# Optimization experiments

Hardware: AMD Instinct MI355X
Metric: run time of the kernel (lower is better)

## Reference

```python
import jax, jax.numpy as jnp
import numpy as np

B, S, H, N = 2, 2048, 1024, 16
D = H // N


def setup_inputs() -> dict:
    key = jax.random.key(0)
    k1, k2, k3 = jax.random.split(key, 3)
    # Xavier-uniform-ish init for projection weights
    lim_in = (6.0 / (H + 3 * H)) ** 0.5
    lim_out = (6.0 / (H + H)) ** 0.5
    return {
        "hidden_states": jax.random.normal(k1, (B, S, H), dtype=jnp.float32),
        "w_in": jax.random.uniform(k2, (3 * H, H), minval=-lim_in, maxval=lim_in, dtype=jnp.float32),
        "b_in": jnp.zeros((3 * H,), dtype=jnp.float32),
        "w_out": jax.random.uniform(k3, (H, H), minval=-lim_out, maxval=lim_out, dtype=jnp.float32),
        "b_out": jnp.zeros((H,), dtype=jnp.float32),
    }


def reference(hidden_states, w_in, b_in, w_out, b_out):
    b, s, h = hidden_states.shape
    qkv = hidden_states @ w_in.T + b_in  # [B,S,3H]
    q, k, v = jnp.split(qkv, 3, axis=-1)
    # [B,S,H] -> [B,N,S,D]
    def to_heads(x):
        return x.reshape(b, s, N, D).transpose(0, 2, 1, 3)
    q, k, v = to_heads(q), to_heads(k), to_heads(v)
    scale = D ** -0.5
    scores = jnp.einsum("bnqd,bnkd->bnqk", q, k) * scale  # [B,N,S,S]
    causal = jnp.triu(jnp.ones((s, s), dtype=bool), k=1)
    scores = jnp.where(causal, -jnp.inf, scores)
    attn = jax.nn.softmax(scores, axis=-1)
    out = jnp.einsum("bnqk,bnkd->bnqd", attn, v)  # [B,N,S,D]
    out = out.transpose(0, 2, 1, 3).reshape(b, s, h)
    return out @ w_out.T + b_out
```

## Files before the change

kernel.cpp:

```cpp
#include <hip/hip_runtime.h>
#include <hip/hip_bf16.h>

#define BB 2
#define SS 2048
#define HH 1024
#define NH 16
#define DD 64
#define H3 3072
#define MM (BB*SS)

typedef unsigned short u16;
typedef unsigned int u32;
typedef __attribute__((ext_vector_type(8))) short bf16x8;
typedef __attribute__((ext_vector_type(4))) float f32x4;

__device__ __forceinline__ u16 f2bf(float f) {
    union { float f; u32 u; } v; v.f = f;
    u32 u = v.u;
    u += 0x7fffu + ((u >> 16) & 1u);
    return (u16)(u >> 16);
}
__device__ __forceinline__ float bf2f(u16 h) {
    union { u32 u; float f; } v; v.u = ((u32)h) << 16;
    return v.f;
}
__device__ __forceinline__ u32 pack2bf(float a, float b) {
    __hip_bfloat162 h = __float22bfloat162_rn(float2{a, b});
    u32 u; __builtin_memcpy(&u, &h, 4);
    return u;
}
__device__ __forceinline__ void gl_lds16(const void* g, void* l) {
    __builtin_amdgcn_global_load_lds(
        (const __attribute__((address_space(1))) u32*)g,
        (__attribute__((address_space(3))) u32*)l, 16, 0, 0);
}

__global__ void cvt2bf(const float4* __restrict__ s0, uint2* __restrict__ d0, int n0,
                       const float4* __restrict__ s1, uint2* __restrict__ d1, int n1) {
    int i = blockIdx.x * blockDim.x + threadIdx.x;
    const int tot = n0 + n1;
    for (; i < tot; i += gridDim.x * blockDim.x) {
        const float4* s = (i < n0) ? s0 : s1;
        uint2* d       = (i < n0) ? d0 : d1;
        int j          = (i < n0) ? i : i - n0;
        float4 v = s[j];
        uint2 o; o.x = pack2bf(v.x, v.y); o.y = pack2bf(v.z, v.w);
        d[j] = o;
    }
}

template<bool ACVT, int BN, int MODE>
__global__ __launch_bounds__(256, 2)
void gemm_k(const void* __restrict__ Aptr, const u16* __restrict__ Bbf,
            const u16* __restrict__ biasbf, void* __restrict__ Cptr,
            u16* __restrict__ qk, u16* __restrict__ vt, int M, int Nn, int K)
{
    constexpr int ASTR = ACVT ? 40 : 32;
    constexpr int NFR  = BN / 32;
    __shared__ __align__(16) u16 Alds[128 * ASTR];
    __shared__ __align__(16) u16 Blds[BN * 32];
    const int tid = threadIdx.x;
    const int w = tid >> 6, lane = tid & 63, quad = lane >> 4, l16 = lane & 15;
    const int m0 = blockIdx.x * 128, n0 = blockIdx.y * BN;
    const int wm = w >> 1, wn = w & 1;
    const int rA = lane >> 3, c4 = (lane & 7) * 4;
    const int rA4 = lane >> 2, c8b = (lane & 3) * 8;

    f32x4 acc[4][NFR] = {};

    for (int k0 = 0; k0 < K; k0 += 32) {
        __syncthreads();
        if constexpr (ACVT) {
            const float* A = (const float*)Aptr;
#pragma unroll
            for (int q = 0; q < 4; ++q) {
                int row = w * 32 + q * 8 + rA;
                float4 v = *(const float4*)&A[(size_t)(m0 + row) * K + k0 + c4];
                u32* dst = (u32*)&Alds[row * ASTR + c4];
                dst[0] = pack2bf(v.x, v.y);
                dst[1] = pack2bf(v.z, v.w);
            }
        } else {
            const u16* A = (const u16*)Aptr;
#pragma unroll
            for (int q = 0; q < 2; ++q) {
                int row0 = w * 32 + q * 16;
                gl_lds16(&A[(size_t)(m0 + row0 + rA4) * K + k0 + c8b],
                         &Alds[row0 * 32]);
            }
        }
#pragma unroll
        for (int q = 0; q < BN / 64; ++q) {
            int row0 = w * (BN / 4) + q * 16;
            gl_lds16(&Bbf[(size_t)(n0 + row0 + rA4) * K + k0 + c8b],
                     &Blds[row0 * 32]);
        }
        __syncthreads();

        bf16x8 af[4], bfr[NFR];
#pragma unroll
        for (int mi = 0; mi < 4; ++mi)
            af[mi] = *(const bf16x8*)&Alds[(wm * 64 + mi * 16 + l16) * ASTR + quad * 8];
#pragma unroll
        for (int ni = 0; ni < NFR; ++ni)
            bfr[ni] = *(const bf16x8*)&Blds[(wn * (BN / 2) + ni * 16 + l16) * 32 + quad * 8];
#pragma unroll
        for (int mi = 0; mi < 4; ++mi)
#pragma unroll
            for (int ni = 0; ni < NFR; ++ni)
                acc[mi][ni] = __builtin_amdgcn_mfma_f32_16x16x32_bf16(
                    af[mi], bfr[ni], acc[mi][ni], 0, 0, 0);
    }

#pragma unroll
    for (int mi = 0; mi < 4; ++mi) {
        int row_b = m0 + wm * 64 + mi * 16 + quad * 4;
#pragma unroll
        for (int ni = 0; ni < NFR; ++ni) {
            int col = n0 + wn * (BN / 2) + ni * 16 + l16;
            float bv = bf2f(biasbf[col]);
            if constexpr (MODE == 1) {
#pragma unroll
                for (int i = 0; i < 4; ++i)
                    ((float*)Cptr)[(size_t)(row_b + i) * Nn + col] = acc[mi][ni][i] + bv;
            } else {
                if (col < 2048) {
                    float sc = (col < 1024) ? 0.125f : 1.0f;
#pragma unroll
                    for (int i = 0; i < 4; ++i)
                        qk[(size_t)(row_b + i) * 2048 + col] = f2bf((acc[mi][ni][i] + bv) * sc);
                } else {
                    int d = col - 2048, hh = d >> 6, dd = d & 63;
                    int b = row_b >> 11, s = row_b & 2047;
                    u16 t0 = f2bf(acc[mi][ni][0] + bv), t1 = f2bf(acc[mi][ni][1] + bv);
                    u16 t2 = f2bf(acc[mi][ni][2] + bv), t3 = f2bf(acc[mi][ni][3] + bv);
                    uint2 pk; pk.x = (u32)t0 | ((u32)t1 << 16);
                    pk.y = (u32)t2 | ((u32)t3 << 16);
                    *(uint2*)&vt[((size_t)((b * 16 + hh) * 64 + dd)) * 2048 + s] = pk;
                }
            }
        }
    }
}

__global__ __launch_bounds__(256, 2)
void attn_v2(const u16* __restrict__ qk, const u16* __restrict__ vt,
             u16* __restrict__ attn_out) {
    const int pr = blockIdx.x, h = blockIdx.y, b = blockIdx.z;
    const int tid = threadIdx.x;
    const int w = tid >> 6, lane = tid & 63, quad = lane >> 4, l16 = lane & 15;
    __shared__ __align__(16) u16 Klds[64 * 72];
    __shared__ __align__(16) u16 Vlds[64 * 72];
    __shared__ __align__(16) u16 Pbuf[64 * 72];
    __shared__ float Lred[4][64];
    __shared__ float Linv[64];

    const int r0 = tid >> 3, cc8 = (tid & 7) * 8;

    for (int half = 0; half < 2; ++half) {
        const int qt = (half == 0) ? (31 - pr) : pr;
        const int q0 = qt * 64;
        const int T = qt + 1;

        bf16x8 qf[4][2];
        {
            const u16* qb = qk + (size_t)(b * SS + q0) * 2048 + h * 64;
#pragma unroll
            for (int mi = 0; mi < 4; ++mi)
#pragma unroll
                for (int kc = 0; kc < 2; ++kc)
                    qf[mi][kc] = *(const bf16x8*)
                        &qb[(size_t)(mi * 16 + l16) * 2048 + kc * 32 + quad * 8];
        }

        const u16* Kg = qk + (size_t)(b * SS) * 2048 + 1024 + h * 64;
        const u16* Vg = vt + (size_t)((b * 16 + h) * 64) * 2048;

        f32x4 oacc[4] = {};
        float l_lane[16];
#pragma unroll
        for (int j = 0; j < 16; ++j) l_lane[j] = 0.f;

        uint4 kr0, kr1, vr0, vr1;
        kr0 = *(const uint4*)&Kg[(size_t)(r0) * 2048 + cc8];
        kr1 = *(const uint4*)&Kg[(size_t)(r0 + 32) * 2048 + cc8];
        vr0 = *(const uint4*)&Vg[(size_t)(r0) * 2048 + cc8];
        vr1 = *(const uint4*)&Vg[(size_t)(r0 + 32) * 2048 + cc8];

        for (int t = 0; t < T; ++t) {
            const int kv0 = t * 64;
            __syncthreads();
            *(uint4*)&Klds[r0 * 72 + cc8]        = kr0;
            *(uint4*)&Klds[(r0 + 32) * 72 + cc8] = kr1;
            *(uint4*)&Vlds[r0 * 72 + cc8]        = vr0;
            *(uint4*)&Vlds[(r0 + 32) * 72 + cc8] = vr1;
            __syncthreads();
            if (t + 1 < T) {
                const int nv = kv0 + 64;
                kr0 = *(const uint4*)&Kg[(size_t)(nv + r0) * 2048 + cc8];
                kr1 = *(const uint4*)&Kg[(size_t)(nv + r0 + 32) * 2048 + cc8];
                vr0 = *(const uint4*)&Vg[(size_t)(r0) * 2048 + nv + cc8];
                vr1 = *(const uint4*)&Vg[(size_t)(r0 + 32) * 2048 + nv + cc8];
            }
            bf16x8 kf0 = *(const bf16x8*)&Klds[(w * 16 + l16) * 72 + quad * 8];
            bf16x8 kf1 = *(const bf16x8*)&Klds[(w * 16 + l16) * 72 + 32 + quad * 8];
            f32x4 sacc[4] = {};
#pragma unroll
            for (int mi = 0; mi < 4; ++mi) {
                sacc[mi] = __builtin_amdgcn_mfma_f32_16x16x32_bf16(qf[mi][0], kf0, sacc[mi], 0, 0, 0);
                sacc[mi] = __builtin_amdgcn_mfma_f32_16x16x32_bf16(qf[mi][1], kf1, sacc[mi], 0, 0, 0);
            }
            const int colg = kv0 + w * 16 + l16;
#pragma unroll
            for (int mi = 0; mi < 4; ++mi) {
#pragma unroll
                for (int i = 0; i < 4; ++i) {
                    int rowg = q0 + mi * 16 + quad * 4 + i;
                    float p = (colg <= rowg) ? __expf(sacc[mi][i]) : 0.f;
                    l_lane[mi * 4 + i] += p;
                    Pbuf[(mi * 16 + quad * 4 + i) * 72 + w * 16 + l16] = f2bf(p);
                }
            }
            __syncthreads();
            bf16x8 vf0 = *(const bf16x8*)&Vlds[(w * 16 + l16) * 72 + quad * 8];
            bf16x8 vf1 = *(const bf16x8*)&Vlds[(w * 16 + l16) * 72 + 32 + quad * 8];
#pragma unroll
            for (int mi = 0; mi < 4; ++mi) {
                bf16x8 pf0 = *(const bf16x8*)&Pbuf[(mi * 16 + l16) * 72 + quad * 8];
                bf16x8 pf1 = *(const bf16x8*)&Pbuf[(mi * 16 + l16) * 72 + 32 + quad * 8];
                oacc[mi] = __builtin_amdgcn_mfma_f32_16x16x32_bf16(pf0, vf0, oacc[mi], 0, 0, 0);
                oacc[mi] = __builtin_amdgcn_mfma_f32_16x16x32_bf16(pf1, vf1, oacc[mi], 0, 0, 0);
            }
        }

#pragma unroll
        for (int j = 0; j < 16; ++j) {
#pragma unroll
            for (int s = 1; s < 16; s <<= 1)
                l_lane[j] += __shfl_xor(l_lane[j], s, 64);
        }
#pragma unroll
        for (int j = 0; j < 16; ++j)
            if (l16 == j) Lred[w][(j >> 2) * 16 + quad * 4 + (j & 3)] = l_lane[j];
        __syncthreads();
        if (w == 0)
            Linv[lane] = 1.0f / (Lred[0][lane] + Lred[1][lane] + Lred[2][lane] + Lred[3][lane]);
        __syncthreads();
        {
            u16* ob = attn_out + (size_t)(b * SS + q0) * 1024 + h * 64 + w * 16 + l16;
#pragma unroll
            for (int mi = 0; mi < 4; ++mi)
#pragma unroll
                for (int i = 0; i < 4; ++i) {
                    int rl = mi * 16 + quad * 4 + i;
                    ob[(size_t)rl * 1024] = f2bf(oacc[mi][i] * Linv[rl]);
                }
        }
        __syncthreads();
    }
}

extern "C" void kernel_launch(void* const* d_in, const int* in_sizes, int n_in,
                              void* d_out, int out_size, void* d_ws, size_t ws_size,
                              hipStream_t stream) {
    const float* hidden = (const float*)d_in[0];
    const float* w_in   = (const float*)d_in[1];
    const float* b_in   = (const float*)d_in[2];
    const float* w_out  = (const float*)d_in[3];
    const float* b_out  = (const float*)d_in[4];
    float* out = (float*)d_out;

    char* ws = (char*)d_ws;
    u16* wi_bf   = (u16*)ws;
    u16* bi_bf   = (u16*)(ws + 6291456);
    u16* attn_ws = (u16*)ws;
    u16* qk      = (u16*)(ws + 8388608);
    u16* wo_bf   = (u16*)(ws + 8388608);
    u16* bo_bf   = (u16*)(ws + 8388608 + 2097152);
    u16* vt      = (u16*)(ws + 25165824);

    cvt2bf<<<dim3(1024), dim3(256), 0, stream>>>(
        (const float4*)w_in, (uint2*)wi_bf, 786432,
        (const float4*)b_in, (uint2*)bi_bf, 768);
    gemm_k<true, 128, 2><<<dim3(32, 24), dim3(256), 0, stream>>>(
        hidden, wi_bf, bi_bf, nullptr, qk, vt, MM, H3, HH);
    attn_v2<<<dim3(16, NH, BB), dim3(256), 0, stream>>>(qk, vt, attn_ws);
    cvt2bf<<<dim3(1024), dim3(256), 0, stream>>>(
        (const float4*)w_out, (uint2*)wo_bf, 262144,
        (const float4*)b_out, (uint2*)bo_bf, 256);
    gemm_k<false, 64, 1><<<dim3(32, 16), dim3(256), 0, stream>>>(
        attn_ws, wo_bf, bo_bf, out, nullptr, nullptr, MM, HH, HH);
}
```

Before: 189.4 us.

## Restructure attention per-wave rows with double-buffered K/V and pre-converted bf16 input

The attention kernel now gives each wave its own 16 query rows across all 64 keys. This makes the row-sum reduction wave-local, removes the cross-wave LDS reduction, and gives each wave a private P buffer, which cuts barriers per tile from two to one. K and V tiles are double-buffered in LDS so the next tile's global loads overlap compute. The hidden states are converted to bf16 up front into the output buffer, so the QKV GEMM can use the async global-to-LDS path, and Q and K are split into separate contiguous buffers. This adds an extra conversion pass and doubles K/V LDS usage.

```diff
diff --git a/kernel.cpp b/kernel.cpp
--- a/kernel.cpp
+++ b/kernel.cpp
@@ -35,72 +35,58 @@
         (__attribute__((address_space(3))) u32*)l, 16, 0, 0);
 }
 
-__global__ void cvt2bf(const float4* __restrict__ s0, uint2* __restrict__ d0, int n0,
-                       const float4* __restrict__ s1, uint2* __restrict__ d1, int n1) {
+__global__ void cvt3bf(const float4* __restrict__ s0, uint2* __restrict__ d0, int n0,
+                       const float4* __restrict__ s1, uint2* __restrict__ d1, int n1,
+                       const float4* __restrict__ s2, uint2* __restrict__ d2, int n2) {
     int i = blockIdx.x * blockDim.x + threadIdx.x;
-    const int tot = n0 + n1;
+    const int tot = n0 + n1 + n2;
     for (; i < tot; i += gridDim.x * blockDim.x) {
-        const float4* s = (i < n0) ? s0 : s1;
-        uint2* d       = (i < n0) ? d0 : d1;
-        int j          = (i < n0) ? i : i - n0;
+        const float4* s; uint2* d; int j;
+        if (i < n0)            { s = s0; d = d0; j = i; }
+        else if (i < n0 + n1)  { s = s1; d = d1; j = i - n0; }
+        else                   { s = s2; d = d2; j = i - n0 - n1; }
         float4 v = s[j];
         uint2 o; o.x = pack2bf(v.x, v.y); o.y = pack2bf(v.z, v.w);
         d[j] = o;
     }
 }
 
-template<bool ACVT, int BN, int MODE>
+template<int BN, int MODE>
 __global__ __launch_bounds__(256, 2)
-void gemm_k(const void* __restrict__ Aptr, const u16* __restrict__ Bbf,
-            const u16* __restrict__ biasbf, void* __restrict__ Cptr,
-            u16* __restrict__ qk, u16* __restrict__ vt, int M, int Nn, int K)
+void gemm_k2(const u16* __restrict__ A, const u16* __restrict__ Bbf,
+             const u16* __restrict__ biasbf, void* __restrict__ Cptr,
+             u16* __restrict__ Qo, u16* __restrict__ Ko, u16* __restrict__ Vto,
+             int M, int Nn, int K)
 {
-    constexpr int ASTR = ACVT ? 40 : 32;
-    constexpr int NFR  = BN / 32;
-    __shared__ __align__(16) u16 Alds[128 * ASTR];
+    constexpr int NFR = BN / 32;
+    __shared__ __align__(16) u16 Alds[128 * 32];
     __shared__ __align__(16) u16 Blds[BN * 32];
     const int tid = threadIdx.x;
     const int w = tid >> 6, lane = tid & 63, quad = lane >> 4, l16 = lane & 15;
     const int m0 = blockIdx.x * 128, n0 = blockIdx.y * BN;
     const int wm = w >> 1, wn = w & 1;
-    const int rA = lane >> 3, c4 = (lane & 7) * 4;
     const int rA4 = lane >> 2, c8b = (lane & 3) * 8;
 
     f32x4 acc[4][NFR] = {};
 
     for (int k0 = 0; k0 < K; k0 += 32) {
         __syncthreads();
-        if constexpr (ACVT) {
-            const float* A = (const float*)Aptr;
-#pragma unroll
-            for (int q = 0; q < 4; ++q) {
-                int row = w * 32 + q * 8 + rA;
-                float4 v = *(const float4*)&A[(size_t)(m0 + row) * K + k0 + c4];
-                u32* dst = (u32*)&Alds[row * ASTR + c4];
-                dst[0] = pack2bf(v.x, v.y);
-                dst[1] = pack2bf(v.z, v.w);
-            }
-        } else {
-            const u16* A = (const u16*)Aptr;
-#pragma unroll
-            for (int q = 0; q < 2; ++q) {
-                int row0 = w * 32 + q * 16;
-                gl_lds16(&A[(size_t)(m0 + row0 + rA4) * K + k0 + c8b],
-                         &Alds[row0 * 32]);
-            }
+#pragma unroll
+        for (int q = 0; q < 2; ++q) {
+            int row0 = w * 32 + q * 16;
+            gl_lds16(&A[(size_t)(m0 + row0 + rA4) * K + k0 + c8b], &Alds[row0 * 32]);
         }
 #pragma unroll
         for (int q = 0; q < BN / 64; ++q) {
             int row0 = w * (BN / 4) + q * 16;
-            gl_lds16(&Bbf[(size_t)(n0 + row0 + rA4) * K + k0 + c8b],
-                     &Blds[row0 * 32]);
+            gl_lds16(&Bbf[(size_t)(n0 + row0 + rA4) * K + k0 + c8b], &Blds[row0 * 32]);
         }
         __syncthreads();
 
         bf16x8 af[4], bfr[NFR];
 #pragma unroll
         for (int mi = 0; mi < 4; ++mi)
-            af[mi] = *(const bf16x8*)&Alds[(wm * 64 + mi * 16 + l16) * ASTR + quad * 8];
+            af[mi] = *(const bf16x8*)&Alds[(wm * 64 + mi * 16 + l16) * 32 + quad * 8];
 #pragma unroll
         for (int ni = 0; ni < NFR; ++ni)
             bfr[ni] = *(const bf16x8*)&Blds[(wn * (BN / 2) + ni * 16 + l16) * 32 + quad * 8];
@@ -124,11 +110,16 @@
                 for (int i = 0; i < 4; ++i)
                     ((float*)Cptr)[(size_t)(row_b + i) * Nn + col] = acc[mi][ni][i] + bv;
             } else {
-                if (col < 2048) {
-                    float sc = (col < 1024) ? 0.125f : 1.0f;
+                if (col < 1024) {
 #pragma unroll
                     for (int i = 0; i < 4; ++i)
-                        qk[(size_t)(row_b + i) * 2048 + col] = f2bf((acc[mi][ni][i] + bv) * sc);
+                        Qo[(size_t)(row_b + i) * 1024 + col] =
+                            f2bf((acc[mi][ni][i] + bv) * 0.125f);
+                } else if (col < 2048) {
+#pragma unroll
+                    for (int i = 0; i < 4; ++i)
+                        Ko[(size_t)(row_b + i) * 1024 + (col - 1024)] =
+                            f2bf(acc[mi][ni][i] + bv);
                 } else {
                     int d = col - 2048, hh = d >> 6, dd = d & 63;
                     int b = row_b >> 11, s = row_b & 2047;
@@ -136,7 +127,7 @@
                     u16 t2 = f2bf(acc[mi][ni][2] + bv), t3 = f2bf(acc[mi][ni][3] + bv);
                     uint2 pk; pk.x = (u32)t0 | ((u32)t1 << 16);
                     pk.y = (u32)t2 | ((u32)t3 << 16);
-                    *(uint2*)&vt[((size_t)((b * 16 + hh) * 64 + dd)) * 2048 + s] = pk;
+                    *(uint2*)&Vto[((size_t)((b * 16 + hh) * 64 + dd)) * 2048 + s] = pk;
                 }
             }
         }
@@ -144,119 +135,103 @@
 }
 
 __global__ __launch_bounds__(256, 2)
-void attn_v2(const u16* __restrict__ qk, const u16* __restrict__ vt,
-             u16* __restrict__ attn_out) {
+void attn_v3(const u16* __restrict__ Q, const u16* __restrict__ Kb,
+             const u16* __restrict__ Vt, u16* __restrict__ attn_out) {
     const int pr = blockIdx.x, h = blockIdx.y, b = blockIdx.z;
     const int tid = threadIdx.x;
     const int w = tid >> 6, lane = tid & 63, quad = lane >> 4, l16 = lane & 15;
-    __shared__ __align__(16) u16 Klds[64 * 72];
-    __shared__ __align__(16) u16 Vlds[64 * 72];
-    __shared__ __align__(16) u16 Pbuf[64 * 72];
-    __shared__ float Lred[4][64];
-    __shared__ float Linv[64];
-
+    __shared__ __align__(16) u16 Klds[2][64 * 72];
+    __shared__ __align__(16) u16 Vlds[2][64 * 72];
+    __shared__ __align__(16) u16 Pb[4][16 * 72];
     const int r0 = tid >> 3, cc8 = (tid & 7) * 8;
 
     for (int half = 0; half < 2; ++half) {
-        const int qt = (half == 0) ? (31 - pr) : pr;
+        const int qt = half ? pr : (31 - pr);
         const int q0 = qt * 64;
         const int T = qt + 1;
 
-        bf16x8 qf[4][2];
-        {
-            const u16* qb = qk + (size_t)(b * SS + q0) * 2048 + h * 64;
-#pragma unroll
-            for (int mi = 0; mi < 4; ++mi)
-#pragma unroll
-                for (int kc = 0; kc < 2; ++kc)
-                    qf[mi][kc] = *(const bf16x8*)
-                        &qb[(size_t)(mi * 16 + l16) * 2048 + kc * 32 + quad * 8];
-        }
-
-        const u16* Kg = qk + (size_t)(b * SS) * 2048 + 1024 + h * 64;
-        const u16* Vg = vt + (size_t)((b * 16 + h) * 64) * 2048;
+        const u16* Qb = Q  + (size_t)(b * SS + q0) * 1024 + h * 64;
+        const u16* Kg = Kb + (size_t)(b * SS) * 1024 + h * 64;
+        const u16* Vg = Vt + (size_t)((b * 16 + h) * 64) * 2048;
+
+        bf16x8 qf0 = *(const bf16x8*)&Qb[(size_t)(w * 16 + l16) * 1024 + quad * 8];
+        bf16x8 qf1 = *(const bf16x8*)&Qb[(size_t)(w * 16 + l16) * 1024 + 32 + quad * 8];
 
         f32x4 oacc[4] = {};
-        float l_lane[16];
-#pragma unroll
-        for (int j = 0; j < 16; ++j) l_lane[j] = 0.f;
-
-        uint4 kr0, kr1, vr0, vr1;
-        kr0 = *(const uint4*)&Kg[(size_t)(r0) * 2048 + cc8];
-        kr1 = *(const uint4*)&Kg[(size_t)(r0 + 32) * 2048 + cc8];
-        vr0 = *(const uint4*)&Vg[(size_t)(r0) * 2048 + cc8];
-        vr1 = *(const uint4*)&Vg[(size_t)(r0 + 32) * 2048 + cc8];
+        float lp[4] = {0.f, 0.f, 0.f, 0.f};
+
+        uint4 kr0 = *(const uint4*)&Kg[(size_t)r0 * 1024 + cc8];
+        uint4 kr1 = *(const uint4*)&Kg[(size_t)(r0 + 32) * 1024 + cc8];
+        uint4 vr0 = *(const uint4*)&Vg[(size_t)r0 * 2048 + cc8];
+        uint4 vr1 = *(const uint4*)&Vg[(size_t)(r0 + 32) * 2048 + cc8];
+        __syncthreads();
+        *(uint4*)&Klds[0][r0 * 72 + cc8]        = kr0;
+        *(uint4*)&Klds[0][(r0 + 32) * 72 + cc8] = kr1;
+        *(uint4*)&Vlds[0][r0 * 72 + cc8]        = vr0;
+        *(uint4*)&Vlds[0][(r0 + 32) * 72 + cc8] = vr1;
 
         for (int t = 0; t < T; ++t) {
-            const int kv0 = t * 64;
-            __syncthreads();
-            *(uint4*)&Klds[r0 * 72 + cc8]        = kr0;
-            *(uint4*)&Klds[(r0 + 32) * 72 + cc8] = kr1;
-            *(uint4*)&Vlds[r0 * 72 + cc8]        = vr0;
-            *(uint4*)&Vlds[(r0 + 32) * 72 + cc8] = vr1;
+            const int cur = t & 1;
             __syncthreads();
             if (t + 1 < T) {
-                const int nv = kv0 + 64;
-                kr0 = *(const uint4*)&Kg[(size_t)(nv + r0) * 2048 + cc8];
-                kr1 = *(const uint4*)&Kg[(size_t)(nv + r0 + 32) * 2048 + cc8];
-                vr0 = *(const uint4*)&Vg[(size_t)(r0) * 2048 + nv + cc8];
+                const int nv = (t + 1) * 64;
+                kr0 = *(const uint4*)&Kg[(size_t)(nv + r0) * 1024 + cc8];
+                kr1 = *(const uint4*)&Kg[(size_t)(nv + r0 + 32) * 1024 + cc8];
+                vr0 = *(const uint4*)&Vg[(size_t)r0 * 2048 + nv + cc8];
                 vr1 = *(const uint4*)&Vg[(size_t)(r0 + 32) * 2048 + nv + cc8];
             }
-            bf16x8 kf0 = *(const bf16x8*)&Klds[(w * 16 + l16) * 72 + quad * 8];
-            bf16x8 kf1 = *(const bf16x8*)&Klds[(w * 16 + l16) * 72 + 32 + quad * 8];
             f32x4 sacc[4] = {};
 #pragma unroll
-            for (int mi = 0; mi < 4; ++mi) {
-                sacc[mi] = __builtin_amdgcn_mfma_f32_16x16x32_bf16(qf[mi][0], kf0, sacc[mi], 0, 0, 0);
-                sacc[mi] = __builtin_amdgcn_mfma_f32_16x16x32_bf16(qf[mi][1], kf1, sacc[mi], 0, 0, 0);
-            }
-            const int colg = kv0 + w * 16 + l16;
-#pragma unroll
-            for (int mi = 0; mi < 4; ++mi) {
+            for (int ni = 0; ni < 4; ++ni) {
+                bf16x8 kf0 = *(const bf16x8*)&Klds[cur][(ni * 16 + l16) * 72 + quad * 8];
+                bf16x8 kf1 = *(const bf16x8*)&Klds[cur][(ni * 16 + l16) * 72 + 32 + quad * 8];
+                sacc[ni] = __builtin_amdgcn_mfma_f32_16x16x32_bf16(qf0, kf0, sacc[ni], 0, 0, 0);
+                sacc[ni] = __builtin_amdgcn_mfma_f32_16x16x32_bf16(qf1, kf1, sacc[ni], 0, 0, 0);
+            }
+            const int kv0 = t * 64;
+#pragma unroll
+            for (int ni = 0; ni < 4; ++ni) {
+                int colg = kv0 + ni * 16 + l16;
 #pragma unroll
                 for (int i = 0; i < 4; ++i) {
-                    int rowg = q0 + mi * 16 + quad * 4 + i;
-                    float p = (colg <= rowg) ? __expf(sacc[mi][i]) : 0.f;
-                    l_lane[mi * 4 + i] += p;
-                    Pbuf[(mi * 16 + quad * 4 + i) * 72 + w * 16 + l16] = f2bf(p);
+                    int rowg = q0 + w * 16 + quad * 4 + i;
+                    float p = (colg <= rowg) ? __expf(sacc[ni][i]) : 0.f;
+                    lp[i] += p;
+                    Pb[w][(quad * 4 + i) * 72 + ni * 16 + l16] = f2bf(p);
                 }
             }
-            __syncthreads();
-            bf16x8 vf0 = *(const bf16x8*)&Vlds[(w * 16 + l16) * 72 + quad * 8];
-            bf16x8 vf1 = *(const bf16x8*)&Vlds[(w * 16 + l16) * 72 + 32 + quad * 8];
-#pragma unroll
-            for (int mi = 0; mi < 4; ++mi) {
-                bf16x8 pf0 = *(const bf16x8*)&Pbuf[(mi * 16 + l16) * 72 + quad * 8];
-                bf16x8 pf1 = *(const bf16x8*)&Pbuf[(mi * 16 + l16) * 72 + 32 + quad * 8];
-                oacc[mi] = __builtin_amdgcn_mfma_f32_16x16x32_bf16(pf0, vf0, oacc[mi], 0, 0, 0);
-                oacc[mi] = __builtin_amdgcn_mfma_f32_16x16x32_bf16(pf1, vf1, oacc[mi], 0, 0, 0);
-            }
-        }
-
-#pragma unroll
-        for (int j = 0; j < 16; ++j) {
+            bf16x8 pf0 = *(const bf16x8*)&Pb[w][l16 * 72 + quad * 8];
+            bf16x8 pf1 = *(const bf16x8*)&Pb[w][l16 * 72 + 32 + quad * 8];
+#pragma unroll
+            for (int ni = 0; ni < 4; ++ni) {
+                bf16x8 vf0 = *(const bf16x8*)&Vlds[cur][(ni * 16 + l16) * 72 + quad * 8];
+                bf16x8 vf1 = *(const bf16x8*)&Vlds[cur][(ni * 16 + l16) * 72 + 32 + quad * 8];
+                oacc[ni] = __builtin_amdgcn_mfma_f32_16x16x32_bf16(pf0, vf0, oacc[ni], 0, 0, 0);
+                oacc[ni] = __builtin_amdgcn_mfma_f32_16x16x32_bf16(pf1, vf1, oacc[ni], 0, 0, 0);
+            }
+            if (t + 1 < T) {
+                const int nxt = cur ^ 1;
+                *(uint4*)&Klds[nxt][r0 * 72 + cc8]        = kr0;
+                *(uint4*)&Klds[nxt][(r0 + 32) * 72 + cc8] = kr1;
+                *(uint4*)&Vlds[nxt][r0 * 72 + cc8]        = vr0;
+                *(uint4*)&Vlds[nxt][(r0 + 32) * 72 + cc8] = vr1;
+            }
+        }
+
+#pragma unroll
+        for (int i = 0; i < 4; ++i) {
 #pragma unroll
             for (int s = 1; s < 16; s <<= 1)
-                l_lane[j] += __shfl_xor(l_lane[j], s, 64);
-        }
-#pragma unroll
-        for (int j = 0; j < 16; ++j)
-            if (l16 == j) Lred[w][(j >> 2) * 16 + quad * 4 + (j & 3)] = l_lane[j];
-        __syncthreads();
-        if (w == 0)
-            Linv[lane] = 1.0f / (Lred[0][lane] + Lred[1][lane] + Lred[2][lane] + Lred[3][lane]);
-        __syncthreads();
-        {
-            u16* ob = attn_out + (size_t)(b * SS + q0) * 1024 + h * 64 + w * 16 + l16;
-#pragma unroll
-            for (int mi = 0; mi < 4; ++mi)
-#pragma unroll
-                for (int i = 0; i < 4; ++i) {
-                    int rl = mi * 16 + quad * 4 + i;
-                    ob[(size_t)rl * 1024] = f2bf(oacc[mi][i] * Linv[rl]);
-                }
-        }
-        __syncthreads();
+                lp[i] += __shfl_xor(lp[i], s, 64);
+            lp[i] = 1.0f / lp[i];
+        }
+        u16* ob = attn_out + (size_t)(b * SS + q0 + w * 16) * 1024 + h * 64;
+#pragma unroll
+        for (int ni = 0; ni < 4; ++ni)
+#pragma unroll
+            for (int i = 0; i < 4; ++i)
+                ob[(size_t)(quad * 4 + i) * 1024 + ni * 16 + l16] =
+                    f2bf(oacc[ni][i] * lp[i]);
     }
 }
 
@@ -271,23 +246,28 @@
     float* out = (float*)d_out;
 
     char* ws = (char*)d_ws;
+    u16* hid_bf  = (u16*)d_out;
     u16* wi_bf   = (u16*)ws;
     u16* bi_bf   = (u16*)(ws + 6291456);
     u16* attn_ws = (u16*)ws;
-    u16* qk      = (u16*)(ws + 8388608);
+    u16* Qbuf    = (u16*)(ws + 8388608);
     u16* wo_bf   = (u16*)(ws + 8388608);
     u16* bo_bf   = (u16*)(ws + 8388608 + 2097152);
-    u16* vt      = (u16*)(ws + 25165824);
-
-    cvt2bf<<<dim3(1024), dim3(256), 0, stream>>>(
-        (const float4*)w_in, (uint2*)wi_bf, 786432,
-        (const float4*)b_in, (uint2*)bi_bf, 768);
-    gemm_k<true, 128, 2><<<dim3(32, 24), dim3(256), 0, stream>>>(
-        hidden, wi_bf, bi_bf, nullptr, qk, vt, MM, H3, HH);
-    attn_v2<<<dim3(16, NH, BB), dim3(256), 0, stream>>>(qk, vt, attn_ws);
-    cvt2bf<<<dim3(1024), dim3(256), 0, stream>>>(
+    u16* Kbuf    = (u16*)(ws + 16777216);
+    u16* Vtbuf   = (u16*)(ws + 25165824);
+
+    cvt3bf<<<dim3(2048), dim3(256), 0, stream>>>(
+        (const float4*)hidden, (uint2*)hid_bf, 1048576,
+        (const float4*)w_in,   (uint2*)wi_bf,  786432,
+        (const float4*)b_in,   (uint2*)bi_bf,  768);
+    gemm_k2<128, 2><<<dim3(32, 24), dim3(256), 0, stream>>>(
+        hid_bf, wi_bf, bi_bf, nullptr, Qbuf, Kbuf, Vtbuf, MM, H3, HH);
+    attn_v3<<<dim3(16, NH, BB), dim3(256), 0, stream>>>(
+        Qbuf, Kbuf, Vtbuf, attn_ws);
+    cvt3bf<<<dim3(512), dim3(256), 0, stream>>>(
         (const float4*)w_out, (uint2*)wo_bf, 262144,
-        (const float4*)b_out, (uint2*)bo_bf, 256);
-    gemm_k<false, 64, 1><<<dim3(32, 16), dim3(256), 0, stream>>>(
-        attn_ws, wo_bf, bo_bf, out, nullptr, nullptr, MM, HH, HH);
-}
+        (const float4*)b_out, (uint2*)bo_bf, 256,
+        nullptr, nullptr, 0);
+    gemm_k2<64, 1><<<dim3(32, 16), dim3(256), 0, stream>>>(
+        attn_ws, wo_bf, bo_bf, out, nullptr, nullptr, nullptr, MM, HH, HH);
+}
```

Measured after the change: 187.0 us. About the same (-1.2%).
